# Kernel optimization log

Hardware: AMD Instinct MI355X
Metric: run time of the kernel (lower is better)

## Reference

```python
import jax, jax.numpy as jnp
import numpy as np
import math

EMB, HEAD, B, S = 1024, 64, 4, 4096

def setup_inputs() -> dict:
    key = jax.random.key(0)
    ks = jax.random.split(key, 7)
    scale = 1.0 / math.sqrt(EMB)
    return {
        "x": jax.random.normal(ks[0], (B, S, EMB), dtype=jnp.float32),
        "Wq": jax.random.uniform(ks[1], (EMB, HEAD), jnp.float32, -scale, scale),
        "bq": jax.random.uniform(ks[2], (HEAD,), jnp.float32, -scale, scale),
        "Wk": jax.random.uniform(ks[3], (EMB, HEAD), jnp.float32, -scale, scale),
        "bk": jax.random.uniform(ks[4], (HEAD,), jnp.float32, -scale, scale),
        "Wv": jax.random.uniform(ks[5], (EMB, HEAD), jnp.float32, -scale, scale),
        "bv": jax.random.uniform(ks[6], (HEAD,), jnp.float32, -scale, scale),
    }

def reference(x, Wq, bq, Wk, bk, Wv, bv):
    # x: [B, S, E]
    q = x @ Wq + bq            # [B, S, H]
    k = x @ Wk + bk
    v = x @ Wv + bv
    scores = jnp.einsum('bqh,bkh->bqk', q, k) / math.sqrt(q.shape[-1])
    # causal mask: position q attends to k <= q
    s = x.shape[1]
    causal = jnp.tril(jnp.ones((s, s), dtype=bool))
    scores = jnp.where(causal, scores, -jnp.inf)
    attn = jax.nn.softmax(scores, axis=-1)
    return jnp.einsum('bqk,bkh->bqh', attn, v)
```

## Files before the change

### kernel.cpp

```cpp
#include <hip/hip_runtime.h>
#include <hip/hip_bf16.h>
#include <math.h>

#define EMB 1024
#define HEAD 64
#define NB 4
#define SEQ 4096
#define MTOT (NB * SEQ)
#define QSCALE (0.125f * 1.44269504088896f)

typedef __attribute__((ext_vector_type(8))) short bf16x8;
typedef __attribute__((ext_vector_type(4))) float f32x4;
typedef __attribute__((ext_vector_type(16))) float f32x16;

static __device__ __forceinline__ unsigned short f2b(float f) {
    union { float f; unsigned u; } v; v.f = f;
    unsigned r = v.u + 0x7FFFu + ((v.u >> 16) & 1u);
    return (unsigned short)(r >> 16);
}
static __device__ __forceinline__ float b2f(unsigned short u) {
    union { unsigned u; float f; } v; v.u = ((unsigned)u) << 16; return v.f;
}
static __device__ __forceinline__ unsigned pk2(float lo, float hi) {
    unsigned r;
    asm("v_cvt_pk_bf16_f32 %0, %1, %2" : "=v"(r) : "v"(lo), "v"(hi));
    return r;
}
static __device__ __forceinline__ void gl2lds(const unsigned short* g, unsigned short* l) {
    __builtin_amdgcn_global_load_lds(
        (__attribute__((address_space(1))) const void*)g,
        (__attribute__((address_space(3))) void*)l, 16, 0, 0);
}

__global__ void wt_kernel(const float* __restrict__ Wq, const float* __restrict__ Wk,
                          const float* __restrict__ Wv, unsigned short* __restrict__ Wt) {
    const int idx = blockIdx.x * 256 + threadIdx.x;
    const int m = idx >> 16;
    const int r = idx & 65535;
    const int n = r >> 10, k = r & 1023;
    const float* W = (m == 0) ? Wq : (m == 1) ? Wk : Wv;
    Wt[idx] = f2b(W[k * HEAD + n]);
}

__global__ __launch_bounds__(256) void proj_kernel(
    const float* __restrict__ x, const unsigned short* __restrict__ Wt3,
    const float* __restrict__ bq, const float* __restrict__ bk,
    const float* __restrict__ bv, unsigned short* __restrict__ qg,
    unsigned short* __restrict__ kg, unsigned short* __restrict__ vt) {
    __shared__ unsigned short Ax[32][72];
    __shared__ unsigned short Wl[192][72];

    const int tid = threadIdx.x;
    const int wave = tid >> 6, lane = tid & 63;
    const int li = lane & 15, lg = lane >> 4;
    const int rbase = blockIdx.x * 32;

    f32x4 acc[2][3];
#pragma unroll
    for (int m = 0; m < 2; ++m)
#pragma unroll
        for (int n = 0; n < 3; ++n) acc[m][n] = (f32x4){0.f, 0.f, 0.f, 0.f};

    const int xr = tid >> 3, xc = (tid & 7) * 8;

    for (int k0 = 0; k0 < EMB; k0 += 64) {
        __syncthreads();
        const float* xp = x + (size_t)(rbase + xr) * EMB + k0 + xc;
        const float4 t0 = *(const float4*)(xp);
        const float4 t1 = *(const float4*)(xp + 4);
        union { bf16x8 v; unsigned u[4]; } pa;
        pa.u[0] = pk2(t0.x, t0.y); pa.u[1] = pk2(t0.z, t0.w);
        pa.u[2] = pk2(t1.x, t1.y); pa.u[3] = pk2(t1.z, t1.w);
        *(bf16x8*)&Ax[xr][xc] = pa.v;
#pragma unroll
        for (int i = 0; i < 6; ++i) {
            const int chunk = tid + 256 * i;
            const int row = chunk >> 3, c8 = (chunk & 7) * 8;
            *(bf16x8*)&Wl[row][c8] = *(const bf16x8*)(Wt3 + (size_t)row * EMB + k0 + c8);
        }
        __syncthreads();

        const bf16x8 a0 = *(const bf16x8*)&Ax[li][lg * 8];
        const bf16x8 a1 = *(const bf16x8*)&Ax[li][32 + lg * 8];
        const bf16x8 a2 = *(const bf16x8*)&Ax[16 + li][lg * 8];
        const bf16x8 a3 = *(const bf16x8*)&Ax[16 + li][32 + lg * 8];
#pragma unroll
        for (int n = 0; n < 3; ++n) {
            const bf16x8 b0 = *(const bf16x8*)&Wl[(wave * 3 + n) * 16 + li][lg * 8];
            const bf16x8 b1 = *(const bf16x8*)&Wl[(wave * 3 + n) * 16 + li][32 + lg * 8];
            acc[0][n] = __builtin_amdgcn_mfma_f32_16x16x32_bf16(a0, b0, acc[0][n], 0, 0, 0);
            acc[0][n] = __builtin_amdgcn_mfma_f32_16x16x32_bf16(a1, b1, acc[0][n], 0, 0, 0);
            acc[1][n] = __builtin_amdgcn_mfma_f32_16x16x32_bf16(a2, b0, acc[1][n], 0, 0, 0);
            acc[1][n] = __builtin_amdgcn_mfma_f32_16x16x32_bf16(a3, b1, acc[1][n], 0, 0, 0);
        }
    }
#pragma unroll
    for (int m = 0; m < 2; ++m)
#pragma unroll
        for (int n = 0; n < 3; ++n) {
            const int f = wave * 3 + n;
            const int mat = f >> 2;
            const int nc = (f & 3) * 16 + li;
            const float bb = (mat == 0) ? bq[nc] : (mat == 1) ? bk[nc] : bv[nc];
#pragma unroll
            for (int r = 0; r < 4; ++r) {
                const int grow = rbase + m * 16 + lg * 4 + r;
                const float val = acc[m][n][r] + bb;
                if (mat == 0) {
                    qg[(size_t)grow * HEAD + nc] = f2b(val * QSCALE);
                } else if (mat == 1) {
                    kg[(size_t)grow * HEAD + nc] = f2b(val);
                } else {
                    const int bi = grow >> 12, si = grow & 4095;
                    vt[((size_t)bi * HEAD + nc) * SEQ + si] = f2b(val);
                }
            }
        }
}

template<int W64, int NWIN>
__global__ __launch_bounds__(256) void attn_kernel(
    const unsigned short* __restrict__ Qg, const unsigned short* __restrict__ Kg,
    const unsigned short* __restrict__ Vtg, unsigned* __restrict__ pO,
    float* __restrict__ pML) {
    __shared__ unsigned short Kl[2][4096];
    __shared__ unsigned short Vl[2][4096];

    const int tid = threadIdx.x;
    const int lane = tid & 63, wv = tid >> 6;
    const int ql = lane & 31, h = lane >> 5;
    const int b = blockIdx.y;
    int qp = 0, off = 0;
    for (;;) {
        const int nwq = (2 * qp + 2 + W64 - 1) / W64;
        if (off + nwq > blockIdx.x) break;
        off += nwq; ++qp;
    }
    const int win = blockIdx.x - off;
    const int t0 = win * W64;
    const int tend_blk0 = 2 * qp + 2;
    const int tend_blk = (t0 + W64 < tend_blk0) ? t0 + W64 : tend_blk0;
    const int qidx = qp * 4 + wv;
    const int tdiag = qidx >> 1;
    const int qa0 = qidx * 32;
    const int myend = (t0 + W64 < tdiag + 1) ? t0 + W64 : tdiag + 1;

    const size_t qb = (size_t)b * SEQ * HEAD;
    const unsigned short* vtb = Vtg + (size_t)b * HEAD * SEQ;

    int krow[2], koff[2];
#pragma unroll
    for (int j = 0; j < 2; ++j) {
        const int chunk = (wv * 2 + j) * 64 + lane;
        krow[j] = chunk >> 3;
        koff[j] = ((chunk & 7) ^ (krow[j] & 7)) << 3;
    }

    const unsigned short* qrow = Qg + qb + (size_t)(qa0 + ql) * HEAD + h * 8;
    bf16x8 qf[4];
#pragma unroll
    for (int s = 0; s < 4; ++s) qf[s] = *(const bf16x8*)(qrow + s * 16);

    f32x16 oa0, oa1;
#pragma unroll
    for (int r = 0; r < 16; ++r) { oa0[r] = 0.f; oa1[r] = 0.f; }
    float m = -1e30f, lsum = 0.f;

    const int sw = (ql & 7) << 4;

#pragma unroll
    for (int j = 0; j < 2; ++j) {
        gl2lds(Kg + qb + (size_t)(t0 * 64 + krow[j]) * HEAD + koff[j], &Kl[0][(wv * 2 + j) * 512]);
        gl2lds(vtb + (size_t)krow[j] * SEQ + t0 * 64 + koff[j], &Vl[0][(wv * 2 + j) * 512]);
    }
    __syncthreads();

    for (int t = t0; t < tend_blk; ++t) {
        const int cur = (t - t0) & 1;
        if (t + 1 < tend_blk) {
            const int kv1 = (t + 1) * 64;
#pragma unroll
            for (int j = 0; j < 2; ++j) {
                gl2lds(Kg + qb + (size_t)(kv1 + krow[j]) * HEAD + koff[j], &Kl[cur ^ 1][(wv * 2 + j) * 512]);
                gl2lds(vtb + (size_t)krow[j] * SEQ + kv1 + koff[j], &Vl[cur ^ 1][(wv * 2 + j) * 512]);
            }
        }
        if (t < myend) {
            const char* kb = (const char*)Kl[cur];
            bf16x8 kf[2][4];
#pragma unroll
            for (int hh = 0; hh < 2; ++hh)
#pragma unroll
                for (int s = 0; s < 4; ++s)
                    kf[hh][s] = *(const bf16x8*)(kb + (hh * 32 + ql) * 128 + ((32 * s + 16 * h) ^ sw));

            f32x16 st0, st1;
#pragma unroll
            for (int r = 0; r < 16; ++r) { st0[r] = 0.f; st1[r] = 0.f; }
            __builtin_amdgcn_s_setprio(1);
#pragma unroll
            for (int s = 0; s < 4; ++s) {
                st0 = __builtin_amdgcn_mfma_f32_32x32x16_bf16(kf[0][s], qf[s], st0, 0, 0, 0);
                st1 = __builtin_amdgcn_mfma_f32_32x32x16_bf16(kf[1][s], qf[s], st1, 0, 0, 0);
            }
            __builtin_amdgcn_s_setprio(0);

            const char* vbp = (const char*)Vl[cur];
            bf16x8 vf[2][4];
#pragma unroll
            for (int dt = 0; dt < 2; ++dt)
#pragma unroll
                for (int cc = 0; cc < 4; ++cc)
                    vf[dt][cc] = *(const bf16x8*)(vbp + (dt * 32 + ql) * 128 + ((32 * cc + 16 * h) ^ sw));

            if (t == tdiag) {
                if (qidx & 1) {
#pragma unroll
                    for (int r = 0; r < 16; ++r) {
                        const int kvl = (r & 3) + 8 * (r >> 2) + 4 * h;
                        if (kvl > ql) st1[r] = -1e30f;
                    }
                } else {
#pragma unroll
                    for (int r = 0; r < 16; ++r) {
                        const int kvl = (r & 3) + 8 * (r >> 2) + 4 * h;
                        if (kvl > ql) st0[r] = -1e30f;
                        st1[r] = -1e30f;
                    }
                }
            }
            float cm = -1e30f;
#pragma unroll
            for (int r = 0; r < 16; ++r) cm = fmaxf(cm, fmaxf(st0[r], st1[r]));
            cm = fmaxf(cm, __shfl_xor(cm, 32));
            if (!__all(cm - m <= 8.0f)) {
                const float mn = fmaxf(m, cm);
                const float sc = exp2f(m - mn);
                m = mn;
                lsum *= sc;
#pragma unroll
                for (int r = 0; r < 16; ++r) { oa0[r] *= sc; oa1[r] *= sc; }
            }
            float ls = 0.f;
#pragma unroll
            for (int r = 0; r < 16; ++r) {
                st0[r] = exp2f(st0[r] - m);
                st1[r] = exp2f(st1[r] - m);
                ls += st0[r] + st1[r];
            }
            lsum += ls;

            bf16x8 bfv[4];
#pragma unroll
            for (int hh = 0; hh < 2; ++hh) {
                unsigned w8[8];
#pragma unroll
                for (int tt = 0; tt < 8; ++tt)
                    w8[tt] = hh ? pk2(st1[2 * tt], st1[2 * tt + 1])
                                : pk2(st0[2 * tt], st0[2 * tt + 1]);
                const unsigned xa0 = h ? w8[0] : w8[2];
                const unsigned va0 = __shfl_xor((int)xa0, 32);
                const unsigned xb0 = h ? w8[1] : w8[3];
                const unsigned vb0 = __shfl_xor((int)xb0, 32);
                union { bf16x8 v; unsigned u[4]; } bb;
                bb.u[0] = h ? va0 : w8[0];
                bb.u[1] = h ? vb0 : w8[1];
                bb.u[2] = h ? w8[2] : va0;
                bb.u[3] = h ? w8[3] : vb0;
                bfv[hh * 2] = bb.v;
                const unsigned xa1 = h ? w8[4] : w8[6];
                const unsigned va1 = __shfl_xor((int)xa1, 32);
                const unsigned xb1 = h ? w8[5] : w8[7];
                const unsigned vb1 = __shfl_xor((int)xb1, 32);
                bb.u[0] = h ? va1 : w8[4];
                bb.u[1] = h ? vb1 : w8[5];
                bb.u[2] = h ? w8[6] : va1;
                bb.u[3] = h ? w8[7] : vb1;
                bfv[hh * 2 + 1] = bb.v;
            }
            __builtin_amdgcn_s_setprio(1);
#pragma unroll
            for (int cc = 0; cc < 4; ++cc) {
                oa0 = __builtin_amdgcn_mfma_f32_32x32x16_bf16(vf[0][cc], bfv[cc], oa0, 0, 0, 0);
                oa1 = __builtin_amdgcn_mfma_f32_32x32x16_bf16(vf[1][cc], bfv[cc], oa1, 0, 0, 0);
            }
            __builtin_amdgcn_s_setprio(0);
        }
        __syncthreads();
    }

    if (t0 <= tdiag) {
        lsum += __shfl_xor(lsum, 32);
        const int Os = 128 * win - W64 * win * (win - 1);
        const size_t gw = (size_t)b * NWIN + Os + (qidx - 2 * W64 * win);
        unsigned* po = pO + gw * 1024;
#pragma unroll
        for (int r = 0; r < 16; r += 2) {
            const int dp = ((r & 3) >> 1) + 4 * (r >> 2) + 2 * h;
            po[dp * 32 + ql] = pk2(oa0[r], oa0[r + 1]);
            po[(16 + dp) * 32 + ql] = pk2(oa1[r], oa1[r + 1]);
        }
        if (h == 0) {
            pML[gw * 64 + ql * 2] = m;
            pML[gw * 64 + ql * 2 + 1] = lsum;
        }
    }
}

template<int W64, int NWIN>
__global__ __launch_bounds__(256) void merge_kernel(
    const unsigned* __restrict__ pO, const float* __restrict__ pML,
    float* __restrict__ out) {
    const int qidx = blockIdx.x, b = blockIdx.y;
    const int wcount = qidx / (2 * W64) + 1;
    const int t = threadIdx.x;
    const int ql = t & 31, g = t >> 5;

    float M = -1e30f;
    for (int k = 0; k < wcount; ++k) {
        const int Os = 128 * k - W64 * k * (k - 1);
        const size_t gw = (size_t)b * NWIN + Os + (qidx - 2 * W64 * k);
        M = fmaxf(M, pML[gw * 64 + ql * 2]);
    }
    float acc[8] = {0.f, 0.f, 0.f, 0.f, 0.f, 0.f, 0.f, 0.f};
    float L = 0.f;
    for (int k = 0; k < wcount; ++k) {
        const int Os = 128 * k - W64 * k * (k - 1);
        const size_t gw = (size_t)b * NWIN + Os + (qidx - 2 * W64 * k);
        const float mk = pML[gw * 64 + ql * 2];
        const float lk = pML[gw * 64 + ql * 2 + 1];
        const float wgt = exp2f(mk - M);
        L += wgt * lk;
#pragma unroll
        for (int i = 0; i < 4; ++i) {
            const unsigned u = pO[gw * 1024 + (size_t)(g * 4 + i) * 32 + ql];
            acc[2 * i] += wgt * b2f((unsigned short)(u & 0xFFFFu));
            acc[2 * i + 1] += wgt * b2f((unsigned short)(u >> 16));
        }
    }
    const float inv = 1.0f / L;
    float* op = out + ((size_t)b * SEQ + qidx * 32 + ql) * HEAD + g * 8;
    f32x4 o0 = {acc[0] * inv, acc[1] * inv, acc[2] * inv, acc[3] * inv};
    f32x4 o1 = {acc[4] * inv, acc[5] * inv, acc[6] * inv, acc[7] * inv};
    *(f32x4*)(op) = o0;
    *(f32x4*)(op + 4) = o1;
}

extern "C" void kernel_launch(void* const* d_in, const int* in_sizes, int n_in,
                              void* d_out, int out_size, void* d_ws, size_t ws_size,
                              hipStream_t stream) {
    const float* x  = (const float*)d_in[0];
    const float* Wq = (const float*)d_in[1];
    const float* bq = (const float*)d_in[2];
    const float* Wk = (const float*)d_in[3];
    const float* bk = (const float*)d_in[4];
    const float* Wv = (const float*)d_in[5];
    const float* bv = (const float*)d_in[6];

    unsigned short* Wt = (unsigned short*)d_ws;
    unsigned short* qg = Wt + 3 * HEAD * EMB;
    unsigned short* kg = qg + (size_t)MTOT * HEAD;
    unsigned short* vt = kg + (size_t)MTOT * HEAD;
    unsigned* pO = (unsigned*)(vt + (size_t)MTOT * HEAD);
    const size_t base_shorts = (size_t)3 * HEAD * EMB + (size_t)3 * MTOT * HEAD;

    wt_kernel<<<dim3(768), dim3(256), 0, stream>>>(Wq, Wk, Wv, Wt);
    proj_kernel<<<dim3(MTOT / 32), dim3(256), 0, stream>>>(x, Wt, bq, bk, bv, qg, kg, vt);

    const size_t need4 = base_shorts * 2 + (size_t)NB * 1088 * (1024 * 4 + 64 * 4);
    if (ws_size >= need4) {
        float* pML = (float*)(pO + (size_t)NB * 1088 * 1024);
        attn_kernel<4, 1088><<<dim3(272, NB), dim3(256), 0, stream>>>(qg, kg, vt, pO, pML);
        merge_kernel<4, 1088><<<dim3(128, NB), dim3(256), 0, stream>>>(pO, pML, (float*)d_out);
    } else {
        float* pML = (float*)(pO + (size_t)NB * 576 * 1024);
        attn_kernel<8, 576><<<dim3(144, NB), dim3(256), 0, stream>>>(qg, kg, vt, pO, pML);
        merge_kernel<8, 576><<<dim3(128, NB), dim3(256), 0, stream>>>(pO, pML, (float*)d_out);
    }
}
```

Baseline: 75.77 us.

## Drop LDS staging in attention; load K/V fragments directly from fragment-major global layout

The projection kernel now writes K and V in a pre-tiled, fragment-major layout so each lane can load its MFMA operands straight from global memory with 16-byte loads. The attention kernel drops the shared-memory double buffer and block-level barriers. Work is assigned per wave rather than per block, and K for the next tile is register-prefetched. This removes LDS traffic and __syncthreads stalls. In exchange, waves in a block that touch the same tiles no longer share them, so more traffic goes through L2, and register pressure rises.

```diff
diff --git a/kernel.cpp b/kernel.cpp
--- a/kernel.cpp
+++ b/kernel.cpp
@@ -25,11 +25,6 @@
     unsigned r;
     asm("v_cvt_pk_bf16_f32 %0, %1, %2" : "=v"(r) : "v"(lo), "v"(hi));
     return r;
-}
-static __device__ __forceinline__ void gl2lds(const unsigned short* g, unsigned short* l) {
-    __builtin_amdgcn_global_load_lds(
-        (__attribute__((address_space(1))) const void*)g,
-        (__attribute__((address_space(3))) void*)l, 16, 0, 0);
 }
 
 __global__ void wt_kernel(const float* __restrict__ Wq, const float* __restrict__ Wk,
@@ -46,7 +41,7 @@
     const float* __restrict__ x, const unsigned short* __restrict__ Wt3,
     const float* __restrict__ bq, const float* __restrict__ bk,
     const float* __restrict__ bv, unsigned short* __restrict__ qg,
-    unsigned short* __restrict__ kg, unsigned short* __restrict__ vt) {
+    unsigned short* __restrict__ kb, unsigned short* __restrict__ vb) {
     __shared__ unsigned short Ax[32][72];
     __shared__ unsigned short Wl[192][72];
 
@@ -106,55 +101,42 @@
             for (int r = 0; r < 4; ++r) {
                 const int grow = rbase + m * 16 + lg * 4 + r;
                 const float val = acc[m][n][r] + bb;
+                const int bi = grow >> 12, si = grow & 4095;
                 if (mat == 0) {
                     qg[(size_t)grow * HEAD + nc] = f2b(val * QSCALE);
                 } else if (mat == 1) {
-                    kg[(size_t)grow * HEAD + nc] = f2b(val);
+                    kb[((size_t)(bi * 2 + ((nc >> 3) & 1)) * 4 + (nc >> 4)) * (SEQ * 8)
+                       + (size_t)si * 8 + (nc & 7)] = f2b(val);
                 } else {
-                    const int bi = grow >> 12, si = grow & 4095;
-                    vt[((size_t)bi * HEAD + nc) * SEQ + si] = f2b(val);
+                    vb[((size_t)(bi * 512 + (si >> 3))) * 512 + (size_t)nc * 8 + (si & 7)] = f2b(val);
                 }
             }
         }
 }
 
-template<int W64, int NWIN>
+template<int W64, int NWIN, int KMAX>
 __global__ __launch_bounds__(256) void attn_kernel(
-    const unsigned short* __restrict__ Qg, const unsigned short* __restrict__ Kg,
-    const unsigned short* __restrict__ Vtg, unsigned* __restrict__ pO,
+    const unsigned short* __restrict__ Qg, const unsigned short* __restrict__ Kb,
+    const unsigned short* __restrict__ Vb, unsigned* __restrict__ pO,
     float* __restrict__ pML) {
-    __shared__ unsigned short Kl[2][4096];
-    __shared__ unsigned short Vl[2][4096];
-
-    const int tid = threadIdx.x;
-    const int lane = tid & 63, wv = tid >> 6;
+    const int lane = threadIdx.x & 63;
     const int ql = lane & 31, h = lane >> 5;
     const int b = blockIdx.y;
-    int qp = 0, off = 0;
-    for (;;) {
-        const int nwq = (2 * qp + 2 + W64 - 1) / W64;
-        if (off + nwq > blockIdx.x) break;
-        off += nwq; ++qp;
-    }
-    const int win = blockIdx.x - off;
-    const int t0 = win * W64;
-    const int tend_blk0 = 2 * qp + 2;
-    const int tend_blk = (t0 + W64 < tend_blk0) ? t0 + W64 : tend_blk0;
-    const int qidx = qp * 4 + wv;
+    const int w = blockIdx.x * 4 + (threadIdx.x >> 6);
+    int seg = 0;
+#pragma unroll
+    for (int kk = 1; kk < KMAX; ++kk)
+        if (w >= 128 * kk - W64 * kk * (kk - 1)) seg = kk;
+    const int Os = 128 * seg - W64 * seg * (seg - 1);
+    const int qidx = 2 * W64 * seg + (w - Os);
     const int tdiag = qidx >> 1;
     const int qa0 = qidx * 32;
-    const int myend = (t0 + W64 < tdiag + 1) ? t0 + W64 : tdiag + 1;
+    const int t0 = W64 * seg;
+    const int tend = (t0 + W64 < tdiag + 1) ? t0 + W64 : tdiag + 1;
 
     const size_t qb = (size_t)b * SEQ * HEAD;
-    const unsigned short* vtb = Vtg + (size_t)b * HEAD * SEQ;
-
-    int krow[2], koff[2];
-#pragma unroll
-    for (int j = 0; j < 2; ++j) {
-        const int chunk = (wv * 2 + j) * 64 + lane;
-        krow[j] = chunk >> 3;
-        koff[j] = ((chunk & 7) ^ (krow[j] & 7)) << 3;
-    }
+    const unsigned short* kb0 = Kb + ((size_t)(b * 2 + h)) * 4 * (SEQ * 8);
+    const unsigned short* vb0 = Vb + (size_t)b * 512 * 512;
 
     const unsigned short* qrow = Qg + qb + (size_t)(qa0 + ql) * HEAD + h * 8;
     bf16x8 qf[4];
@@ -166,144 +148,135 @@
     for (int r = 0; r < 16; ++r) { oa0[r] = 0.f; oa1[r] = 0.f; }
     float m = -1e30f, lsum = 0.f;
 
-    const int sw = (ql & 7) << 4;
-
-#pragma unroll
-    for (int j = 0; j < 2; ++j) {
-        gl2lds(Kg + qb + (size_t)(t0 * 64 + krow[j]) * HEAD + koff[j], &Kl[0][(wv * 2 + j) * 512]);
-        gl2lds(vtb + (size_t)krow[j] * SEQ + t0 * 64 + koff[j], &Vl[0][(wv * 2 + j) * 512]);
-    }
-    __syncthreads();
-
-    for (int t = t0; t < tend_blk; ++t) {
-        const int cur = (t - t0) & 1;
-        if (t + 1 < tend_blk) {
-            const int kv1 = (t + 1) * 64;
-#pragma unroll
-            for (int j = 0; j < 2; ++j) {
-                gl2lds(Kg + qb + (size_t)(kv1 + krow[j]) * HEAD + koff[j], &Kl[cur ^ 1][(wv * 2 + j) * 512]);
-                gl2lds(vtb + (size_t)krow[j] * SEQ + kv1 + koff[j], &Vl[cur ^ 1][(wv * 2 + j) * 512]);
-            }
-        }
-        if (t < myend) {
-            const char* kb = (const char*)Kl[cur];
-            bf16x8 kf[2][4];
+    bf16x8 kcur[2][4], knxt[2][4];
+#pragma unroll
+    for (int hh = 0; hh < 2; ++hh)
+#pragma unroll
+        for (int s = 0; s < 4; ++s)
+            kcur[hh][s] = *(const bf16x8*)(kb0 + (size_t)s * (SEQ * 8)
+                                           + ((size_t)t0 * 64 + 32 * hh + ql) * 8);
+
+    for (int t = t0; t < tend; ++t) {
+        bf16x8 vf[2][4];
+#pragma unroll
+        for (int dt = 0; dt < 2; ++dt)
+#pragma unroll
+            for (int cc = 0; cc < 4; ++cc)
+                vf[dt][cc] = *(const bf16x8*)(vb0 + ((size_t)t * 8 + 2 * cc + h) * 512
+                                              + (dt * 32 + ql) * 8);
+
+        f32x16 st0, st1;
+#pragma unroll
+        for (int r = 0; r < 16; ++r) { st0[r] = 0.f; st1[r] = 0.f; }
+        __builtin_amdgcn_s_setprio(1);
+#pragma unroll
+        for (int s = 0; s < 4; ++s) {
+            st0 = __builtin_amdgcn_mfma_f32_32x32x16_bf16(kcur[0][s], qf[s], st0, 0, 0, 0);
+            st1 = __builtin_amdgcn_mfma_f32_32x32x16_bf16(kcur[1][s], qf[s], st1, 0, 0, 0);
+        }
+        __builtin_amdgcn_s_setprio(0);
+
+        if (t + 1 < tend) {
 #pragma unroll
             for (int hh = 0; hh < 2; ++hh)
 #pragma unroll
                 for (int s = 0; s < 4; ++s)
-                    kf[hh][s] = *(const bf16x8*)(kb + (hh * 32 + ql) * 128 + ((32 * s + 16 * h) ^ sw));
-
-            f32x16 st0, st1;
-#pragma unroll
-            for (int r = 0; r < 16; ++r) { st0[r] = 0.f; st1[r] = 0.f; }
-            __builtin_amdgcn_s_setprio(1);
-#pragma unroll
-            for (int s = 0; s < 4; ++s) {
-                st0 = __builtin_amdgcn_mfma_f32_32x32x16_bf16(kf[0][s], qf[s], st0, 0, 0, 0);
-                st1 = __builtin_amdgcn_mfma_f32_32x32x16_bf16(kf[1][s], qf[s], st1, 0, 0, 0);
-            }
-            __builtin_amdgcn_s_setprio(0);
-
-            const char* vbp = (const char*)Vl[cur];
-            bf16x8 vf[2][4];
-#pragma unroll
-            for (int dt = 0; dt < 2; ++dt)
-#pragma unroll
-                for (int cc = 0; cc < 4; ++cc)
-                    vf[dt][cc] = *(const bf16x8*)(vbp + (dt * 32 + ql) * 128 + ((32 * cc + 16 * h) ^ sw));
-
-            if (t == tdiag) {
-                if (qidx & 1) {
-#pragma unroll
-                    for (int r = 0; r < 16; ++r) {
-                        const int kvl = (r & 3) + 8 * (r >> 2) + 4 * h;
-                        if (kvl > ql) st1[r] = -1e30f;
-                    }
-                } else {
-#pragma unroll
-                    for (int r = 0; r < 16; ++r) {
-                        const int kvl = (r & 3) + 8 * (r >> 2) + 4 * h;
-                        if (kvl > ql) st0[r] = -1e30f;
-                        st1[r] = -1e30f;
-                    }
+                    knxt[hh][s] = *(const bf16x8*)(kb0 + (size_t)s * (SEQ * 8)
+                                                   + ((size_t)(t + 1) * 64 + 32 * hh + ql) * 8);
+        }
+
+        if (t == tdiag) {
+            if (qidx & 1) {
+#pragma unroll
+                for (int r = 0; r < 16; ++r) {
+                    const int kvl = (r & 3) + 8 * (r >> 2) + 4 * h;
+                    if (kvl > ql) st1[r] = -1e30f;
+                }
+            } else {
+#pragma unroll
+                for (int r = 0; r < 16; ++r) {
+                    const int kvl = (r & 3) + 8 * (r >> 2) + 4 * h;
+                    if (kvl > ql) st0[r] = -1e30f;
+                    st1[r] = -1e30f;
                 }
             }
-            float cm = -1e30f;
-#pragma unroll
-            for (int r = 0; r < 16; ++r) cm = fmaxf(cm, fmaxf(st0[r], st1[r]));
-            cm = fmaxf(cm, __shfl_xor(cm, 32));
-            if (!__all(cm - m <= 8.0f)) {
-                const float mn = fmaxf(m, cm);
-                const float sc = exp2f(m - mn);
-                m = mn;
-                lsum *= sc;
-#pragma unroll
-                for (int r = 0; r < 16; ++r) { oa0[r] *= sc; oa1[r] *= sc; }
-            }
-            float ls = 0.f;
-#pragma unroll
-            for (int r = 0; r < 16; ++r) {
-                st0[r] = exp2f(st0[r] - m);
-                st1[r] = exp2f(st1[r] - m);
-                ls += st0[r] + st1[r];
-            }
-            lsum += ls;
-
-            bf16x8 bfv[4];
-#pragma unroll
-            for (int hh = 0; hh < 2; ++hh) {
-                unsigned w8[8];
-#pragma unroll
-                for (int tt = 0; tt < 8; ++tt)
-                    w8[tt] = hh ? pk2(st1[2 * tt], st1[2 * tt + 1])
-                                : pk2(st0[2 * tt], st0[2 * tt + 1]);
-                const unsigned xa0 = h ? w8[0] : w8[2];
-                const unsigned va0 = __shfl_xor((int)xa0, 32);
-                const unsigned xb0 = h ? w8[1] : w8[3];
-                const unsigned vb0 = __shfl_xor((int)xb0, 32);
-                union { bf16x8 v; unsigned u[4]; } bb;
-                bb.u[0] = h ? va0 : w8[0];
-                bb.u[1] = h ? vb0 : w8[1];
-                bb.u[2] = h ? w8[2] : va0;
-                bb.u[3] = h ? w8[3] : vb0;
-                bfv[hh * 2] = bb.v;
-                const unsigned xa1 = h ? w8[4] : w8[6];
-                const unsigned va1 = __shfl_xor((int)xa1, 32);
-                const unsigned xb1 = h ? w8[5] : w8[7];
-                const unsigned vb1 = __shfl_xor((int)xb1, 32);
-                bb.u[0] = h ? va1 : w8[4];
-                bb.u[1] = h ? vb1 : w8[5];
-                bb.u[2] = h ? w8[6] : va1;
-                bb.u[3] = h ? w8[7] : vb1;
-                bfv[hh * 2 + 1] = bb.v;
-            }
-            __builtin_amdgcn_s_setprio(1);
-#pragma unroll
-            for (int cc = 0; cc < 4; ++cc) {
-                oa0 = __builtin_amdgcn_mfma_f32_32x32x16_bf16(vf[0][cc], bfv[cc], oa0, 0, 0, 0);
-                oa1 = __builtin_amdgcn_mfma_f32_32x32x16_bf16(vf[1][cc], bfv[cc], oa1, 0, 0, 0);
-            }
-            __builtin_amdgcn_s_setprio(0);
-        }
-        __syncthreads();
-    }
-
-    if (t0 <= tdiag) {
-        lsum += __shfl_xor(lsum, 32);
-        const int Os = 128 * win - W64 * win * (win - 1);
-        const size_t gw = (size_t)b * NWIN + Os + (qidx - 2 * W64 * win);
-        unsigned* po = pO + gw * 1024;
-#pragma unroll
-        for (int r = 0; r < 16; r += 2) {
-            const int dp = ((r & 3) >> 1) + 4 * (r >> 2) + 2 * h;
-            po[dp * 32 + ql] = pk2(oa0[r], oa0[r + 1]);
-            po[(16 + dp) * 32 + ql] = pk2(oa1[r], oa1[r + 1]);
-        }
-        if (h == 0) {
-            pML[gw * 64 + ql * 2] = m;
-            pML[gw * 64 + ql * 2 + 1] = lsum;
-        }
+        }
+        float cm = -1e30f;
+#pragma unroll
+        for (int r = 0; r < 16; ++r) cm = fmaxf(cm, fmaxf(st0[r], st1[r]));
+        cm = fmaxf(cm, __shfl_xor(cm, 32));
+        if (!__all(cm - m <= 8.0f)) {
+            const float mn = fmaxf(m, cm);
+            const float sc = exp2f(m - mn);
+            m = mn;
+            lsum *= sc;
+#pragma unroll
+            for (int r = 0; r < 16; ++r) { oa0[r] *= sc; oa1[r] *= sc; }
+        }
+        float ls = 0.f;
+#pragma unroll
+        for (int r = 0; r < 16; ++r) {
+            st0[r] = exp2f(st0[r] - m);
+            st1[r] = exp2f(st1[r] - m);
+            ls += st0[r] + st1[r];
+        }
+        lsum += ls;
+
+        bf16x8 bfv[4];
+#pragma unroll
+        for (int hh = 0; hh < 2; ++hh) {
+            unsigned w8[8];
+#pragma unroll
+            for (int tt = 0; tt < 8; ++tt)
+                w8[tt] = hh ? pk2(st1[2 * tt], st1[2 * tt + 1])
+                            : pk2(st0[2 * tt], st0[2 * tt + 1]);
+            const unsigned xa0 = h ? w8[0] : w8[2];
+            const unsigned va0 = __shfl_xor((int)xa0, 32);
+            const unsigned xb0 = h ? w8[1] : w8[3];
+            const unsigned vb_0 = __shfl_xor((int)xb0, 32);
+            union { bf16x8 v; unsigned u[4]; } bbv;
+            bbv.u[0] = h ? va0 : w8[0];
+            bbv.u[1] = h ? vb_0 : w8[1];
+            bbv.u[2] = h ? w8[2] : va0;
+            bbv.u[3] = h ? w8[3] : vb_0;
+            bfv[hh * 2] = bbv.v;
+            const unsigned xa1 = h ? w8[4] : w8[6];
+            const unsigned va1 = __shfl_xor((int)xa1, 32);
+            const unsigned xb1 = h ? w8[5] : w8[7];
+            const unsigned vb_1 = __shfl_xor((int)xb1, 32);
+            bbv.u[0] = h ? va1 : w8[4];
+            bbv.u[1] = h ? vb_1 : w8[5];
+            bbv.u[2] = h ? w8[6] : va1;
+            bbv.u[3] = h ? w8[7] : vb_1;
+            bfv[hh * 2 + 1] = bbv.v;
+        }
+        __builtin_amdgcn_s_setprio(1);
+#pragma unroll
+        for (int cc = 0; cc < 4; ++cc) {
+            oa0 = __builtin_amdgcn_mfma_f32_32x32x16_bf16(vf[0][cc], bfv[cc], oa0, 0, 0, 0);
+            oa1 = __builtin_amdgcn_mfma_f32_32x32x16_bf16(vf[1][cc], bfv[cc], oa1, 0, 0, 0);
+        }
+        __builtin_amdgcn_s_setprio(0);
+
+#pragma unroll
+        for (int hh = 0; hh < 2; ++hh)
+#pragma unroll
+            for (int s = 0; s < 4; ++s)
+                kcur[hh][s] = knxt[hh][s];
+    }
+
+    lsum += __shfl_xor(lsum, 32);
+    const size_t gw = (size_t)b * NWIN + w;
+    unsigned* po = pO + gw * 1024;
+#pragma unroll
+    for (int r = 0; r < 16; r += 2) {
+        const int dp = ((r & 3) >> 1) + 4 * (r >> 2) + 2 * h;
+        po[dp * 32 + ql] = pk2(oa0[r], oa0[r + 1]);
+        po[(16 + dp) * 32 + ql] = pk2(oa1[r], oa1[r + 1]);
+    }
+    if (h == 0) {
+        pML[gw * 64 + ql * 2] = m;
+        pML[gw * 64 + ql * 2 + 1] = lsum;
     }
 }
 
@@ -359,22 +332,22 @@
 
     unsigned short* Wt = (unsigned short*)d_ws;
     unsigned short* qg = Wt + 3 * HEAD * EMB;
-    unsigned short* kg = qg + (size_t)MTOT * HEAD;
-    unsigned short* vt = kg + (size_t)MTOT * HEAD;
-    unsigned* pO = (unsigned*)(vt + (size_t)MTOT * HEAD);
+    unsigned short* kb = qg + (size_t)MTOT * HEAD;
+    unsigned short* vb = kb + (size_t)MTOT * HEAD;
+    unsigned* pO = (unsigned*)(vb + (size_t)MTOT * HEAD);
     const size_t base_shorts = (size_t)3 * HEAD * EMB + (size_t)3 * MTOT * HEAD;
 
     wt_kernel<<<dim3(768), dim3(256), 0, stream>>>(Wq, Wk, Wv, Wt);
-    proj_kernel<<<dim3(MTOT / 32), dim3(256), 0, stream>>>(x, Wt, bq, bk, bv, qg, kg, vt);
+    proj_kernel<<<dim3(MTOT / 32), dim3(256), 0, stream>>>(x, Wt, bq, bk, bv, qg, kb, vb);
 
     const size_t need4 = base_shorts * 2 + (size_t)NB * 1088 * (1024 * 4 + 64 * 4);
     if (ws_size >= need4) {
         float* pML = (float*)(pO + (size_t)NB * 1088 * 1024);
-        attn_kernel<4, 1088><<<dim3(272, NB), dim3(256), 0, stream>>>(qg, kg, vt, pO, pML);
+        attn_kernel<4, 1088, 16><<<dim3(272, NB), dim3(256), 0, stream>>>(qg, kb, vb, pO, pML);
         merge_kernel<4, 1088><<<dim3(128, NB), dim3(256), 0, stream>>>(pO, pML, (float*)d_out);
     } else {
         float* pML = (float*)(pO + (size_t)NB * 576 * 1024);
-        attn_kernel<8, 576><<<dim3(144, NB), dim3(256), 0, stream>>>(qg, kg, vt, pO, pML);
+        attn_kernel<8, 576, 8><<<dim3(144, NB), dim3(256), 0, stream>>>(qg, kb, vb, pO, pML);
         merge_kernel<8, 576><<<dim3(128, NB), dim3(256), 0, stream>>>(pO, pML, (float*)d_out);
     }
 }
```

New measurement: 72.09 us. 1.05x faster.
